# Optimization experiments

Measured on AMD Instinct MI355X. Metric: run time of the kernel, lower is better.

The kernel has to match this reference:

```python
import jax, jax.numpy as jnp
import numpy as np

D_MODEL = 1024
EXPAND = 2
D_INNER = D_MODEL * EXPAND
KERNEL = 4
EPS = 1e-5


def setup_inputs() -> dict:
    key = jax.random.key(0)
    ks = jax.random.split(key, 8)
    B, L = 2, 4096
    x = jax.random.normal(ks[0], (B, L, D_MODEL), dtype=jnp.float32)
    norm_w = jnp.ones((D_MODEL,), jnp.float32)
    norm_b = jnp.zeros((D_MODEL,), jnp.float32)
    # torch Linear weight layout [out, in]
    in_proj_w = jax.random.normal(ks[1], (2 * D_INNER, D_MODEL), jnp.float32) / np.sqrt(D_MODEL)
    # depthwise Conv1d weight [d_inner, 1, K]
    conv_w = jax.random.normal(ks[2], (D_INNER, 1, KERNEL), jnp.float32) / np.sqrt(KERNEL)
    conv_b = jax.random.normal(ks[3], (D_INNER,), jnp.float32) * 0.02
    gate_w = jax.random.normal(ks[4], (D_INNER, D_INNER), jnp.float32) / np.sqrt(D_INNER)
    gate_b = jnp.zeros((D_INNER,), jnp.float32)
    out_proj_w = jax.random.normal(ks[5], (D_MODEL, D_INNER), jnp.float32) / np.sqrt(D_INNER)
    return {"x": x, "norm_w": norm_w, "norm_b": norm_b, "in_proj_w": in_proj_w,
            "conv_w": conv_w, "conv_b": conv_b, "gate_w": gate_w, "gate_b": gate_b,
            "out_proj_w": out_proj_w}


def _layernorm(x, w, b):
    mu = jnp.mean(x, axis=-1, keepdims=True)
    var = jnp.var(x, axis=-1, keepdims=True)
    return (x - mu) * jax.lax.rsqrt(var + EPS) * w + b


def _glru(x, norm_w, norm_b, in_proj_w, conv_w, conv_b, gate_w, gate_b, out_proj_w):
    B, L, D = x.shape
    residual = x
    xn = _layernorm(x, norm_w, norm_b)
    xz = jnp.einsum('bld,ed->ble', xn, in_proj_w)  # [B,L,2*d_inner]
    x_inner, z = jnp.split(xz, 2, axis=-1)
    # causal depthwise conv: torch pads 3 both sides then slices [:L] == left-pad 3
    lhs = jnp.transpose(x_inner, (0, 2, 1))  # [B, C, L]
    conv = jax.lax.conv_general_dilated(
        lhs, conv_w, window_strides=(1,), padding=[(KERNEL - 1, 0)],
        feature_group_count=D_INNER,
        dimension_numbers=('NCH', 'OIH', 'NCH'))
    x_conv = jnp.transpose(conv, (0, 2, 1)) + conv_b  # [B, L, C]
    x_conv = jax.nn.silu(x_conv)
    a = jax.nn.sigmoid(jnp.einsum('blc,ec->ble', x_conv, gate_w) + gate_b)
    b = (1.0 - a) * x_conv
    # h_t = a_t * h_{t-1} + b_t, h_0 prior = 0 -> parallel associative scan
    def combine(e1, e2):
        a1, b1 = e1
        a2, b2 = e2
        return a1 * a2, a2 * b1 + b2
    _, y = jax.lax.associative_scan(combine, (a, b), axis=1)
    y = y * jax.nn.silu(z)
    return residual + jnp.einsum('blc,dc->bld', y, out_proj_w)


def reference(x, norm_w, norm_b, in_proj_w, conv_w, conv_b, gate_w, gate_b, out_proj_w):
    return _glru(x, norm_w, norm_b, in_proj_w, conv_w, conv_b, gate_w, gate_b, out_proj_w)
```

## Files before the change

kernel.cpp:

```cpp
#include <hip/hip_runtime.h>
#include <cstdint>

#define D_MODEL 1024
#define D_INNER 2048
#define LSEQ    4096
#define BATCH   2
#define M_ROWS  (BATCH * LSEQ)
#define CHUNK   128
#define NCHUNK  (LSEQ / CHUNK)

typedef unsigned short u16;
typedef __bf16 bf16x8 __attribute__((ext_vector_type(8)));
typedef float f32x4 __attribute__((ext_vector_type(4)));
typedef u16 u16x4 __attribute__((ext_vector_type(4)));

__device__ __forceinline__ u16 f2bf(float f) {
  union { float f; unsigned u; } x; x.f = f;
  unsigned u = x.u;
  unsigned r = (u + 0x7FFFu + ((u >> 16) & 1u)) >> 16;
  return (u16)r;
}
__device__ __forceinline__ float bf2f(u16 h) {
  union { unsigned u; float f; } x; x.u = ((unsigned)h) << 16;
  return x.f;
}
__device__ __forceinline__ float sigmoidf_(float v) { return 1.0f / (1.0f + expf(-v)); }
__device__ __forceinline__ float siluf_(float v)    { return v / (1.0f + expf(-v)); }

__device__ __forceinline__ void gl_lds16(const void* g, void* l) {
  __builtin_amdgcn_global_load_lds(
      (const __attribute__((address_space(1))) void*)g,
      (__attribute__((address_space(3))) void*)l, 16, 0, 0);
}

#define SBAR()   asm volatile("s_barrier" ::: "memory")
#define WAITV0() asm volatile("s_waitcnt vmcnt(0)" ::: "memory")

__global__ void __launch_bounds__(256)
cast_bf16_kernel(const float* __restrict__ in, u16* __restrict__ out, int n4) {
  int i = blockIdx.x * 256 + threadIdx.x;
  if (i < n4) {
    float4 v = ((const float4*)in)[i];
    u16x4 o;
    o.x = f2bf(v.x); o.y = f2bf(v.y); o.z = f2bf(v.z); o.w = f2bf(v.w);
    ((u16x4*)out)[i] = o;
  }
}

__global__ void __launch_bounds__(256)
ln_kernel(const float* __restrict__ x, const float* __restrict__ w,
          const float* __restrict__ b, u16* __restrict__ xn) {
  const int row = blockIdx.x;
  const int t = threadIdx.x;
  const float4 v = ((const float4*)(x + (size_t)row * D_MODEL))[t];
  float s  = v.x + v.y + v.z + v.w;
  float ss = v.x * v.x + v.y * v.y + v.z * v.z + v.w * v.w;
#pragma unroll
  for (int o = 32; o > 0; o >>= 1) {
    s  += __shfl_xor(s, o);
    ss += __shfl_xor(ss, o);
  }
  __shared__ float red[8];
  const int wid = t >> 6, lane = t & 63;
  if (lane == 0) { red[wid] = s; red[4 + wid] = ss; }
  __syncthreads();
  s  = red[0] + red[1] + red[2] + red[3];
  ss = red[4] + red[5] + red[6] + red[7];
  const float mu  = s * (1.0f / D_MODEL);
  const float var = ss * (1.0f / D_MODEL) - mu * mu;
  const float rs  = rsqrtf(var + 1e-5f);
  const float4 wv = ((const float4*)w)[t];
  const float4 bv = ((const float4*)b)[t];
  u16x4 o4;
  o4.x = f2bf((v.x - mu) * rs * wv.x + bv.x);
  o4.y = f2bf((v.y - mu) * rs * wv.y + bv.y);
  o4.z = f2bf((v.z - mu) * rs * wv.z + bv.z);
  o4.w = f2bf((v.w - mu) * rs * wv.w + bv.w);
  ((u16x4*)(xn + (size_t)row * D_MODEL))[t] = o4;
}

#define MFMA_BF16 __builtin_amdgcn_mfma_f32_16x16x32_bf16

template<int EPI, int BN>
__global__ void __launch_bounds__(512)
gemmK(const u16* __restrict__ A, const u16* __restrict__ Bm,
      int M, int N, int K,
      const float* __restrict__ ef, float* __restrict__ of,
      u16* __restrict__ ob0, u16* __restrict__ ob1) {
  constexpr int NI    = BN / 64;
  constexpr int LB    = BN / 128;
  constexpr int BHALF = BN * 64;
  constexpr int BUFS  = 32768 + 2 * BHALF;
  __shared__ __align__(1024) char lds[2 * BUFS];
  const int tid  = threadIdx.x;
  const int wid  = tid >> 6, lane = tid & 63;
  const int nbx  = N / BN;
  const int nwg  = nbx * (M >> 8);
  const int bid  = blockIdx.x;
  const int cpx  = nwg >> 3;
  const int swz  = (bid & 7) * cpx + (bid >> 3);
  const int bx   = swz % nbx, by = swz / nbx;
  const size_t m0 = (size_t)by << 8;
  const size_t n0 = (size_t)bx * BN;

  const int wr = wid >> 2, wc = wid & 3;
  const size_t rb  = (size_t)K * 2;
  const size_t rj16 = 16 * rb;

  const char* gAs = (const char*)A  + (m0 + (size_t)(wid * 32 + (lane >> 2))) * rb + ((lane & 3) << 4);
  const char* gBs = (const char*)Bm + (n0 + (size_t)(wid * 16 * LB + (lane >> 2))) * rb + ((lane & 3) << 4);
  const int sA = wid * 2048;
  const int sB = wid * (LB * 1024);

  const int q = lane >> 4, r15 = lane & 15;
  const int aoff = (wr * 128 + r15) * 64 + q * 16;
  const int boff = (wc * (BN / 4) + r15) * 64 + q * 16;

  f32x4 acc[8][NI] = {};
  const int nk = K >> 6;

#pragma unroll
  for (int kkh = 0; kkh < 2; ++kkh) {
#pragma unroll
    for (int j = 0; j < 2; ++j)
      gl_lds16(gAs + kkh * 64 + j * rj16, lds + kkh * 16384 + sA + j * 1024);
#pragma unroll
    for (int j = 0; j < LB; ++j)
      gl_lds16(gBs + kkh * 64 + j * rj16, lds + 32768 + kkh * BHALF + sB + j * 1024);
  }
  WAITV0();
  SBAR();

  size_t kb = 128;
  for (int t = 0; t < nk; ++t) {
    const int cur = t & 1;
    const char* cb = lds + cur * BUFS;
    char* nbb = lds + (cur ^ 1) * BUFS;
    const bool pf = (t + 1 < nk);
    bf16x8 af[4], bf0[NI], bf1[NI];

    if (pf) {
      gl_lds16(gAs + kb,        nbb + sA);
      gl_lds16(gAs + kb + rj16, nbb + sA + 1024);
    }
#pragma unroll
    for (int mi = 0; mi < 4; ++mi) af[mi] = *(const bf16x8*)(cb + aoff + mi * 1024);
#pragma unroll
    for (int ni = 0; ni < NI; ++ni) bf0[ni] = *(const bf16x8*)(cb + 32768 + boff + ni * 1024);
    __builtin_amdgcn_s_setprio(1);
#pragma unroll
    for (int mi = 0; mi < 4; ++mi)
#pragma unroll
      for (int ni = 0; ni < NI; ++ni)
        acc[mi][ni] = MFMA_BF16(af[mi], bf0[ni], acc[mi][ni], 0, 0, 0);
    __builtin_amdgcn_s_setprio(0);

    if (pf) {
#pragma unroll
      for (int j = 0; j < LB; ++j)
        gl_lds16(gBs + kb + j * rj16, nbb + 32768 + sB + j * 1024);
    }
#pragma unroll
    for (int mi = 0; mi < 4; ++mi) af[mi] = *(const bf16x8*)(cb + 4096 + aoff + mi * 1024);
    if (pf) {
      if constexpr (LB == 2) asm volatile("s_waitcnt vmcnt(4)" ::: "memory");
      else                   asm volatile("s_waitcnt vmcnt(3)" ::: "memory");
    } else {
      WAITV0();
    }
    SBAR();
    __builtin_amdgcn_s_setprio(1);
#pragma unroll
    for (int mi = 0; mi < 4; ++mi)
#pragma unroll
      for (int ni = 0; ni < NI; ++ni)
        acc[4 + mi][ni] = MFMA_BF16(af[mi], bf0[ni], acc[4 + mi][ni], 0, 0, 0);
    __builtin_amdgcn_s_setprio(0);

    if (pf) {
      gl_lds16(gAs + kb + 64,        nbb + 16384 + sA);
      gl_lds16(gAs + kb + 64 + rj16, nbb + 16384 + sA + 1024);
    }
#pragma unroll
    for (int mi = 0; mi < 4; ++mi) af[mi] = *(const bf16x8*)(cb + 16384 + aoff + mi * 1024);
#pragma unroll
    for (int ni = 0; ni < NI; ++ni) bf1[ni] = *(const bf16x8*)(cb + 32768 + BHALF + boff + ni * 1024);
    __builtin_amdgcn_s_setprio(1);
#pragma unroll
    for (int mi = 0; mi < 4; ++mi)
#pragma unroll
      for (int ni = 0; ni < NI; ++ni)
        acc[mi][ni] = MFMA_BF16(af[mi], bf1[ni], acc[mi][ni], 0, 0, 0);
    __builtin_amdgcn_s_setprio(0);

    if (pf) {
#pragma unroll
      for (int j = 0; j < LB; ++j)
        gl_lds16(gBs + kb + 64 + j * rj16, nbb + 32768 + BHALF + sB + j * 1024);
    }
#pragma unroll
    for (int mi = 0; mi < 4; ++mi) af[mi] = *(const bf16x8*)(cb + 16384 + 4096 + aoff + mi * 1024);
    if (pf) {
      if constexpr (LB == 2) asm volatile("s_waitcnt vmcnt(4)" ::: "memory");
      else                   asm volatile("s_waitcnt vmcnt(3)" ::: "memory");
    }
    SBAR();
    __builtin_amdgcn_s_setprio(1);
#pragma unroll
    for (int mi = 0; mi < 4; ++mi)
#pragma unroll
      for (int ni = 0; ni < NI; ++ni)
        acc[4 + mi][ni] = MFMA_BF16(af[mi], bf1[ni], acc[4 + mi][ni], 0, 0, 0);
    __builtin_amdgcn_s_setprio(0);
    kb += 128;
  }

  const int c0 = lane & 15;
  const int r0 = (lane >> 4) << 2;
  const bool isz = (EPI == 0) && (n0 >= (size_t)D_INNER);
#pragma unroll
  for (int ai = 0; ai < 8; ++ai) {
#pragma unroll
    for (int ni = 0; ni < NI; ++ni) {
#pragma unroll
      for (int rg = 0; rg < 4; ++rg) {
        const size_t row = m0 + (size_t)(wr * 128 + ai * 16 + r0 + rg);
        const size_t col = n0 + (size_t)(wc * (BN / 4) + ni * 16 + c0);
        const float v = acc[ai][ni][rg];
        if (EPI == 0) {
          if (!isz) ob0[row * D_INNER + col] = f2bf(v);
          else      ob1[row * D_INNER + (col - D_INNER)] = f2bf(siluf_(v));
        } else if (EPI == 1) {
          ob0[row * (size_t)N + col] = f2bf(v);
        } else {
          of[row * (size_t)N + col] = v + ef[row * (size_t)N + col];
        }
      }
    }
  }
}

__global__ void __launch_bounds__(256)
conv_silu_kernel(const u16* __restrict__ xin, const float* __restrict__ cw,
                 const float* __restrict__ cb, u16* __restrict__ xc) {
  const int c   = blockIdx.x * 256 + threadIdx.x;
  const int l0  = blockIdx.y * 8;
  const int bat = blockIdx.z;
  const size_t base = ((size_t)bat * LSEQ) * D_INNER + c;
  const float w0 = cw[c * 4 + 0], w1 = cw[c * 4 + 1], w2 = cw[c * 4 + 2], w3 = cw[c * 4 + 3];
  const float bb = cb[c];
  float v[11];
#pragma unroll
  for (int i = 0; i < 11; ++i) {
    const int l = l0 - 3 + i;
    v[i] = (l >= 0) ? bf2f(xin[base + (size_t)l * D_INNER]) : 0.0f;
  }
#pragma unroll
  for (int r = 0; r < 8; ++r) {
    const float acc = bb + w0 * v[r] + w1 * v[r + 1] + w2 * v[r + 2] + w3 * v[r + 3];
    xc[base + (size_t)(l0 + r) * D_INNER] = f2bf(siluf_(acc));
  }
}

__global__ void __launch_bounds__(256)
scan_a_kernel(const u16* __restrict__ g, const u16* __restrict__ xc,
              const float* __restrict__ gbias,
              float* __restrict__ cA, float* __restrict__ cB) {
  const int c   = (blockIdx.x * 256 + threadIdx.x) * 2;
  const int ch  = blockIdx.y;
  const int bat = blockIdx.z;
  const float bb0 = gbias[c], bb1 = gbias[c + 1];
  size_t idx = ((size_t)bat * LSEQ + (size_t)ch * CHUNK) * D_INNER + c;
  float pA0 = 1.0f, hB0 = 0.0f, pA1 = 1.0f, hB1 = 0.0f;
  for (int t = 0; t < CHUNK; ++t) {
    const ushort2 gg = *(const ushort2*)(g + idx);
    const ushort2 xx = *(const ushort2*)(xc + idx);
    const float a0 = sigmoidf_(bf2f(gg.x) + bb0);
    const float a1 = sigmoidf_(bf2f(gg.y) + bb1);
    pA0 *= a0; hB0 = a0 * hB0 + (1.0f - a0) * bf2f(xx.x);
    pA1 *= a1; hB1 = a1 * hB1 + (1.0f - a1) * bf2f(xx.y);
    idx += D_INNER;
  }
  const size_t o = ((size_t)bat * NCHUNK + ch) * D_INNER + c;
  *(float2*)(cA + o) = make_float2(pA0, pA1);
  *(float2*)(cB + o) = make_float2(hB0, hB1);
}

__global__ void __launch_bounds__(256)
scan_b_kernel(const float* __restrict__ cA, const float* __restrict__ cB,
              float* __restrict__ carry) {
  const int tid = blockIdx.x * 256 + threadIdx.x;
  const int bat = tid >> 11;
  const int c   = tid & (D_INNER - 1);
  float h = 0.0f;
  const size_t base = (size_t)bat * NCHUNK * D_INNER + c;
  for (int i = 0; i < NCHUNK; ++i) {
    const size_t o = base + (size_t)i * D_INNER;
    carry[o] = h;
    h = cA[o] * h + cB[o];
  }
}

__global__ void __launch_bounds__(256)
scan_c_kernel(const u16* __restrict__ g, const u16* __restrict__ xc,
              const u16* __restrict__ sz, const float* __restrict__ gbias,
              const float* __restrict__ carry, u16* __restrict__ yg) {
  const int c   = (blockIdx.x * 256 + threadIdx.x) * 2;
  const int ch  = blockIdx.y;
  const int bat = blockIdx.z;
  const float bb0 = gbias[c], bb1 = gbias[c + 1];
  const float2 h2 = *(const float2*)(carry + ((size_t)bat * NCHUNK + ch) * D_INNER + c);
  float h0 = h2.x, h1 = h2.y;
  size_t idx = ((size_t)bat * LSEQ + (size_t)ch * CHUNK) * D_INNER + c;
  for (int t = 0; t < CHUNK; ++t) {
    const ushort2 gg = *(const ushort2*)(g + idx);
    const ushort2 xx = *(const ushort2*)(xc + idx);
    const ushort2 zz = *(const ushort2*)(sz + idx);
    const float a0 = sigmoidf_(bf2f(gg.x) + bb0);
    const float a1 = sigmoidf_(bf2f(gg.y) + bb1);
    h0 = a0 * h0 + (1.0f - a0) * bf2f(xx.x);
    h1 = a1 * h1 + (1.0f - a1) * bf2f(xx.y);
    ushort2 o2;
    o2.x = f2bf(h0 * bf2f(zz.x));
    o2.y = f2bf(h1 * bf2f(zz.y));
    *(ushort2*)(yg + idx) = o2;
    idx += D_INNER;
  }
}

extern "C" void kernel_launch(void* const* d_in, const int* in_sizes, int n_in,
                              void* d_out, int out_size, void* d_ws, size_t ws_size,
                              hipStream_t stream) {
  const float* x         = (const float*)d_in[0];
  const float* norm_w    = (const float*)d_in[1];
  const float* norm_b    = (const float*)d_in[2];
  const float* in_proj_w = (const float*)d_in[3];
  const float* conv_w    = (const float*)d_in[4];
  const float* conv_b    = (const float*)d_in[5];
  const float* gate_w    = (const float*)d_in[6];
  const float* gate_b    = (const float*)d_in[7];
  const float* out_proj_w= (const float*)d_in[8];
  float* out = (float*)d_out;

  char* p = (char*)d_ws;
  u16* xn      = (u16*)p; p += (size_t)M_ROWS * D_MODEL * 2;
  u16* w_in    = (u16*)p; p += (size_t)2 * D_INNER * D_MODEL * 2;
  u16* w_gate  = (u16*)p; p += (size_t)D_INNER * D_INNER * 2;
  u16* w_out   = (u16*)p; p += (size_t)D_MODEL * D_INNER * 2;
  u16* x_inner = (u16*)p; p += (size_t)M_ROWS * D_INNER * 2;
  u16* szb     = (u16*)p; p += (size_t)M_ROWS * D_INNER * 2;
  u16* xconv   = (u16*)p; p += (size_t)M_ROWS * D_INNER * 2;
  u16* gbuf    = (u16*)p; p += (size_t)M_ROWS * D_INNER * 2;
  u16* yg      = (u16*)p; p += (size_t)M_ROWS * D_INNER * 2;
  float* cA    = (float*)p; p += (size_t)BATCH * NCHUNK * D_INNER * 4;
  float* cB    = (float*)p; p += (size_t)BATCH * NCHUNK * D_INNER * 4;
  float* carry = (float*)p; p += (size_t)BATCH * NCHUNK * D_INNER * 4;
  if ((size_t)(p - (char*)d_ws) > ws_size) return;

  cast_bf16_kernel<<<dim3(2 * D_INNER * D_MODEL / 4 / 256), 256, 0, stream>>>(in_proj_w, w_in, 2 * D_INNER * D_MODEL / 4);
  cast_bf16_kernel<<<dim3(D_INNER * D_INNER / 4 / 256), 256, 0, stream>>>(gate_w, w_gate, D_INNER * D_INNER / 4);
  cast_bf16_kernel<<<dim3(D_MODEL * D_INNER / 4 / 256), 256, 0, stream>>>(out_proj_w, w_out, D_MODEL * D_INNER / 4);

  ln_kernel<<<dim3(M_ROWS), 256, 0, stream>>>(x, norm_w, norm_b, xn);

  gemmK<0, 256><<<dim3((M_ROWS / 256) * (2 * D_INNER / 256)), 512, 0, stream>>>(
      xn, w_in, M_ROWS, 2 * D_INNER, D_MODEL, nullptr, nullptr, x_inner, szb);

  conv_silu_kernel<<<dim3(D_INNER / 256, LSEQ / 8, BATCH), 256, 0, stream>>>(x_inner, conv_w, conv_b, xconv);

  gemmK<1, 256><<<dim3((M_ROWS / 256) * (D_INNER / 256)), 512, 0, stream>>>(
      xconv, w_gate, M_ROWS, D_INNER, D_INNER, nullptr, nullptr, gbuf, nullptr);

  scan_a_kernel<<<dim3(D_INNER / 512, NCHUNK, BATCH), 256, 0, stream>>>(gbuf, xconv, gate_b, cA, cB);
  scan_b_kernel<<<dim3(BATCH * D_INNER / 256), 256, 0, stream>>>(cA, cB, carry);
  scan_c_kernel<<<dim3(D_INNER / 512, NCHUNK, BATCH), 256, 0, stream>>>(gbuf, xconv, szb, gate_b, carry, yg);

  gemmK<2, 128><<<dim3((M_ROWS / 256) * (D_MODEL / 128)), 512, 0, stream>>>(
      yg, w_out, M_ROWS, D_MODEL, D_INNER, x, out, nullptr, nullptr);
}
```

Before: 343.1 us.

## Rewrite GEMM with 32x32x16 MFMA, 4 waves, swizzled LDS and register double-buffering

Replaces the 8-wave GEMM built on 16x16x32 bf16 MFMA with a 4-wave kernel that uses 32x32x16 MFMA. Each wave owns a larger 128xBN/2 output tile. The LDS layout uses an XOR swizzle on 16-byte chunks to avoid bank conflicts, and A/B fragments are double-buffered in registers so LDS reads overlap the MFMAs. The aim is more MFMA work per LDS byte and fewer barriers, at the cost of lower occupancy (one block of 256 threads per CU, 256 accumulator floats per thread) and possible register pressure.

```diff
diff --git a/kernel.cpp b/kernel.cpp
--- a/kernel.cpp
+++ b/kernel.cpp
@@ -11,7 +11,7 @@
 
 typedef unsigned short u16;
 typedef __bf16 bf16x8 __attribute__((ext_vector_type(8)));
-typedef float f32x4 __attribute__((ext_vector_type(4)));
+typedef float f32x16 __attribute__((ext_vector_type(16)));
 typedef u16 u16x4 __attribute__((ext_vector_type(4)));
 
 __device__ __forceinline__ u16 f2bf(float f) {
@@ -79,161 +79,150 @@
   ((u16x4*)(xn + (size_t)row * D_MODEL))[t] = o4;
 }
 
-#define MFMA_BF16 __builtin_amdgcn_mfma_f32_16x16x32_bf16
-
 template<int EPI, int BN>
-__global__ void __launch_bounds__(512)
-gemmK(const u16* __restrict__ A, const u16* __restrict__ Bm,
+__global__ void __launch_bounds__(256, 1)
+gemmW(const u16* __restrict__ A, const u16* __restrict__ Bm,
       int M, int N, int K,
       const float* __restrict__ ef, float* __restrict__ of,
       u16* __restrict__ ob0, u16* __restrict__ ob1) {
-  constexpr int NI    = BN / 64;
-  constexpr int LB    = BN / 128;
-  constexpr int BHALF = BN * 64;
-  constexpr int BUFS  = 32768 + 2 * BHALF;
-  __shared__ __align__(1024) char lds[2 * BUFS];
+  constexpr int NF     = BN / 64;
+  constexpr int NBS    = BN / 32;
+  constexpr int BBYTES = BN * 128;
+  __shared__ __align__(1024) char lds[65536 + 2 * BBYTES];
   const int tid  = threadIdx.x;
   const int wid  = tid >> 6, lane = tid & 63;
   const int nbx  = N / BN;
   const int nwg  = nbx * (M >> 8);
   const int bid  = blockIdx.x;
   const int cpx  = nwg >> 3;
-  const int swz  = (bid & 7) * cpx + (bid >> 3);
-  const int bx   = swz % nbx, by = swz / nbx;
+  const int swzb = (bid & 7) * cpx + (bid >> 3);
+  const int bx   = swzb % nbx, by = swzb / nbx;
   const size_t m0 = (size_t)by << 8;
   const size_t n0 = (size_t)bx * BN;
-
-  const int wr = wid >> 2, wc = wid & 3;
+  const int widm = wid >> 1, widn = wid & 1;
   const size_t rb  = (size_t)K * 2;
-  const size_t rj16 = 16 * rb;
-
-  const char* gAs = (const char*)A  + (m0 + (size_t)(wid * 32 + (lane >> 2))) * rb + ((lane & 3) << 4);
-  const char* gBs = (const char*)Bm + (n0 + (size_t)(wid * 16 * LB + (lane >> 2))) * rb + ((lane & 3) << 4);
-  const int sA = wid * 2048;
-  const int sB = wid * (LB * 1024);
-
-  const int q = lane >> 4, r15 = lane & 15;
-  const int aoff = (wr * 128 + r15) * 64 + q * 16;
-  const int boff = (wc * (BN / 4) + r15) * 64 + q * 16;
-
-  f32x4 acc[8][NI] = {};
+  const size_t rj8 = 8 * rb;
+
+  const int sr = lane >> 3;
+  const int ss = ((lane & 7) ^ sr) << 4;
+  const char* gAs = (const char*)A  + (m0 + (size_t)(wid * 64 + sr)) * rb + ss;
+  const char* gBs = (const char*)Bm + (n0 + (size_t)(wid * (BN / 4) + sr)) * rb + ss;
+  const int sAo = wid * 8192;
+  const int sBo = wid * (BN * 32);
+
+  const int l31  = lane & 31;
+  const int hi16 = (lane >> 5) << 4;
+  const int sx   = (lane & 7) << 4;
+  const int arow = (widm * 128 + l31) * 128;
+  const int brow = (widn * (BN / 2) + l31) * 128;
+
+  f32x16 acc[4][NF] = {};
+
+  auto LDA = [&](bf16x8 (&d)[4], const char* Ab, int kk) {
+    const int ko = ((kk * 32) | hi16) ^ sx;
+#pragma unroll
+    for (int mi = 0; mi < 4; ++mi)
+      d[mi] = *(const bf16x8*)(Ab + arow + mi * 4096 + ko);
+  };
+  auto LDB = [&](bf16x8 (&d)[NF], const char* Bb, int kk) {
+    const int ko = ((kk * 32) | hi16) ^ sx;
+#pragma unroll
+    for (int ni = 0; ni < NF; ++ni)
+      d[ni] = *(const bf16x8*)(Bb + brow + ni * 4096 + ko);
+  };
+  auto MM = [&](bf16x8 (&a)[4], bf16x8 (&b)[NF]) {
+#pragma unroll
+    for (int mi = 0; mi < 4; ++mi)
+#pragma unroll
+      for (int ni = 0; ni < NF; ++ni)
+        acc[mi][ni] = __builtin_amdgcn_mfma_f32_32x32x16_bf16(a[mi], b[ni], acc[mi][ni], 0, 0, 0);
+  };
+
   const int nk = K >> 6;
 
 #pragma unroll
-  for (int kkh = 0; kkh < 2; ++kkh) {
-#pragma unroll
-    for (int j = 0; j < 2; ++j)
-      gl_lds16(gAs + kkh * 64 + j * rj16, lds + kkh * 16384 + sA + j * 1024);
-#pragma unroll
-    for (int j = 0; j < LB; ++j)
-      gl_lds16(gBs + kkh * 64 + j * rj16, lds + 32768 + kkh * BHALF + sB + j * 1024);
-  }
+  for (int j = 0; j < 8; ++j)   gl_lds16(gAs + (size_t)j * rj8, lds + sAo + j * 1024);
+#pragma unroll
+  for (int j = 0; j < NBS; ++j) gl_lds16(gBs + (size_t)j * rj8, lds + 65536 + sBo + j * 1024);
   WAITV0();
   SBAR();
+
+  bf16x8 aE[4], bE[NF], aO[4], bO[NF];
+  LDA(aE, lds, 0); LDB(bE, lds + 65536, 0);
 
   size_t kb = 128;
   for (int t = 0; t < nk; ++t) {
     const int cur = t & 1;
-    const char* cb = lds + cur * BUFS;
-    char* nbb = lds + (cur ^ 1) * BUFS;
+    const char* Ac = lds + cur * 32768;
+    const char* Bc = lds + 65536 + cur * BBYTES;
+    char* An = lds + (cur ^ 1) * 32768;
+    char* Bn = lds + 65536 + (cur ^ 1) * BBYTES;
     const bool pf = (t + 1 < nk);
-    bf16x8 af[4], bf0[NI], bf1[NI];
-
+
+    LDA(aO, Ac, 1); LDB(bO, Bc, 1);
     if (pf) {
-      gl_lds16(gAs + kb,        nbb + sA);
-      gl_lds16(gAs + kb + rj16, nbb + sA + 1024);
-    }
-#pragma unroll
-    for (int mi = 0; mi < 4; ++mi) af[mi] = *(const bf16x8*)(cb + aoff + mi * 1024);
-#pragma unroll
-    for (int ni = 0; ni < NI; ++ni) bf0[ni] = *(const bf16x8*)(cb + 32768 + boff + ni * 1024);
-    __builtin_amdgcn_s_setprio(1);
-#pragma unroll
-    for (int mi = 0; mi < 4; ++mi)
-#pragma unroll
-      for (int ni = 0; ni < NI; ++ni)
-        acc[mi][ni] = MFMA_BF16(af[mi], bf0[ni], acc[mi][ni], 0, 0, 0);
-    __builtin_amdgcn_s_setprio(0);
-
+      gl_lds16(gAs + kb,            An + sAo);
+      gl_lds16(gAs + kb + rj8,      An + sAo + 1024);
+      gl_lds16(gAs + kb + 2 * rj8,  An + sAo + 2048);
+      gl_lds16(gBs + kb,            Bn + sBo);
+      gl_lds16(gBs + kb + rj8,      Bn + sBo + 1024);
+    }
+    MM(aE, bE);
+
+    LDA(aE, Ac, 2); LDB(bE, Bc, 2);
     if (pf) {
-#pragma unroll
-      for (int j = 0; j < LB; ++j)
-        gl_lds16(gBs + kb + j * rj16, nbb + 32768 + sB + j * 1024);
-    }
-#pragma unroll
-    for (int mi = 0; mi < 4; ++mi) af[mi] = *(const bf16x8*)(cb + 4096 + aoff + mi * 1024);
+      gl_lds16(gAs + kb + 3 * rj8,  An + sAo + 3072);
+      gl_lds16(gAs + kb + 4 * rj8,  An + sAo + 4096);
+      gl_lds16(gAs + kb + 5 * rj8,  An + sAo + 5120);
+      gl_lds16(gBs + kb + 2 * rj8,  Bn + sBo + 2048);
+      gl_lds16(gBs + kb + 3 * rj8,  Bn + sBo + 3072);
+    }
+    MM(aO, bO);
+
+    LDA(aO, Ac, 3); LDB(bO, Bc, 3);
     if (pf) {
-      if constexpr (LB == 2) asm volatile("s_waitcnt vmcnt(4)" ::: "memory");
-      else                   asm volatile("s_waitcnt vmcnt(3)" ::: "memory");
-    } else {
+      gl_lds16(gAs + kb + 6 * rj8,  An + sAo + 6144);
+      gl_lds16(gAs + kb + 7 * rj8,  An + sAo + 7168);
+      if constexpr (NBS == 8) {
+        gl_lds16(gBs + kb + 4 * rj8, Bn + sBo + 4096);
+        gl_lds16(gBs + kb + 5 * rj8, Bn + sBo + 5120);
+        gl_lds16(gBs + kb + 6 * rj8, Bn + sBo + 6144);
+        gl_lds16(gBs + kb + 7 * rj8, Bn + sBo + 7168);
+      }
+    }
+    MM(aE, bE);
+
+    MM(aO, bO);
+    if (pf) {
       WAITV0();
-    }
-    SBAR();
-    __builtin_amdgcn_s_setprio(1);
-#pragma unroll
-    for (int mi = 0; mi < 4; ++mi)
-#pragma unroll
-      for (int ni = 0; ni < NI; ++ni)
-        acc[4 + mi][ni] = MFMA_BF16(af[mi], bf0[ni], acc[4 + mi][ni], 0, 0, 0);
-    __builtin_amdgcn_s_setprio(0);
-
-    if (pf) {
-      gl_lds16(gAs + kb + 64,        nbb + 16384 + sA);
-      gl_lds16(gAs + kb + 64 + rj16, nbb + 16384 + sA + 1024);
-    }
-#pragma unroll
-    for (int mi = 0; mi < 4; ++mi) af[mi] = *(const bf16x8*)(cb + 16384 + aoff + mi * 1024);
-#pragma unroll
-    for (int ni = 0; ni < NI; ++ni) bf1[ni] = *(const bf16x8*)(cb + 32768 + BHALF + boff + ni * 1024);
-    __builtin_amdgcn_s_setprio(1);
-#pragma unroll
-    for (int mi = 0; mi < 4; ++mi)
-#pragma unroll
-      for (int ni = 0; ni < NI; ++ni)
-        acc[mi][ni] = MFMA_BF16(af[mi], bf1[ni], acc[mi][ni], 0, 0, 0);
-    __builtin_amdgcn_s_setprio(0);
-
-    if (pf) {
-#pragma unroll
-      for (int j = 0; j < LB; ++j)
-        gl_lds16(gBs + kb + 64 + j * rj16, nbb + 32768 + BHALF + sB + j * 1024);
-    }
-#pragma unroll
-    for (int mi = 0; mi < 4; ++mi) af[mi] = *(const bf16x8*)(cb + 16384 + 4096 + aoff + mi * 1024);
-    if (pf) {
-      if constexpr (LB == 2) asm volatile("s_waitcnt vmcnt(4)" ::: "memory");
-      else                   asm volatile("s_waitcnt vmcnt(3)" ::: "memory");
-    }
-    SBAR();
-    __builtin_amdgcn_s_setprio(1);
-#pragma unroll
-    for (int mi = 0; mi < 4; ++mi)
-#pragma unroll
-      for (int ni = 0; ni < NI; ++ni)
-        acc[4 + mi][ni] = MFMA_BF16(af[mi], bf1[ni], acc[4 + mi][ni], 0, 0, 0);
-    __builtin_amdgcn_s_setprio(0);
+      SBAR();
+      LDA(aE, An, 0); LDB(bE, Bn, 0);
+    }
     kb += 128;
   }
 
-  const int c0 = lane & 15;
-  const int r0 = (lane >> 4) << 2;
+  const int ccol = lane & 31;
+  const int rh   = (lane >> 5) << 2;
   const bool isz = (EPI == 0) && (n0 >= (size_t)D_INNER);
 #pragma unroll
-  for (int ai = 0; ai < 8; ++ai) {
-#pragma unroll
-    for (int ni = 0; ni < NI; ++ni) {
-#pragma unroll
-      for (int rg = 0; rg < 4; ++rg) {
-        const size_t row = m0 + (size_t)(wr * 128 + ai * 16 + r0 + rg);
-        const size_t col = n0 + (size_t)(wc * (BN / 4) + ni * 16 + c0);
-        const float v = acc[ai][ni][rg];
-        if (EPI == 0) {
-          if (!isz) ob0[row * D_INNER + col] = f2bf(v);
-          else      ob1[row * D_INNER + (col - D_INNER)] = f2bf(siluf_(v));
-        } else if (EPI == 1) {
-          ob0[row * (size_t)N + col] = f2bf(v);
-        } else {
-          of[row * (size_t)N + col] = v + ef[row * (size_t)N + col];
+  for (int mi = 0; mi < 4; ++mi) {
+#pragma unroll
+    for (int ni = 0; ni < NF; ++ni) {
+#pragma unroll
+      for (int g = 0; g < 4; ++g) {
+#pragma unroll
+        for (int r = 0; r < 4; ++r) {
+          const float v = acc[mi][ni][g * 4 + r];
+          const size_t row = m0 + (size_t)(widm * 128 + mi * 32 + g * 8 + r + rh);
+          const size_t col = n0 + (size_t)(widn * (BN / 2) + ni * 32 + ccol);
+          if (EPI == 0) {
+            if (!isz) ob0[row * D_INNER + col] = f2bf(v);
+            else      ob1[row * D_INNER + (col - D_INNER)] = f2bf(siluf_(v));
+          } else if (EPI == 1) {
+            ob0[row * (size_t)N + col] = f2bf(v);
+          } else {
+            of[row * (size_t)N + col] = v + ef[row * (size_t)N + col];
+          }
         }
       }
     }
@@ -363,18 +352,18 @@
 
   ln_kernel<<<dim3(M_ROWS), 256, 0, stream>>>(x, norm_w, norm_b, xn);
 
-  gemmK<0, 256><<<dim3((M_ROWS / 256) * (2 * D_INNER / 256)), 512, 0, stream>>>(
+  gemmW<0, 256><<<dim3((M_ROWS / 256) * (2 * D_INNER / 256)), 256, 0, stream>>>(
       xn, w_in, M_ROWS, 2 * D_INNER, D_MODEL, nullptr, nullptr, x_inner, szb);
 
   conv_silu_kernel<<<dim3(D_INNER / 256, LSEQ / 8, BATCH), 256, 0, stream>>>(x_inner, conv_w, conv_b, xconv);
 
-  gemmK<1, 256><<<dim3((M_ROWS / 256) * (D_INNER / 256)), 512, 0, stream>>>(
+  gemmW<1, 256><<<dim3((M_ROWS / 256) * (D_INNER / 256)), 256, 0, stream>>>(
       xconv, w_gate, M_ROWS, D_INNER, D_INNER, nullptr, nullptr, gbuf, nullptr);
 
   scan_a_kernel<<<dim3(D_INNER / 512, NCHUNK, BATCH), 256, 0, stream>>>(gbuf, xconv, gate_b, cA, cB);
   scan_b_kernel<<<dim3(BATCH * D_INNER / 256), 256, 0, stream>>>(cA, cB, carry);
   scan_c_kernel<<<dim3(D_INNER / 512, NCHUNK, BATCH), 256, 0, stream>>>(gbuf, xconv, szb, gate_b, carry, yg);
 
-  gemmK<2, 128><<<dim3((M_ROWS / 256) * (D_MODEL / 128)), 512, 0, stream>>>(
+  gemmW<2, 128><<<dim3((M_ROWS / 256) * (D_MODEL / 128)), 256, 0, stream>>>(
       yg, w_out, M_ROWS, D_MODEL, D_INNER, x, out, nullptr, nullptr);
 }
```

New measurement: 389.7 us. 1.14x slower.
